# Kernel optimization log

Measured on AMD Instinct MI355X. Metric: run time of the kernel, lower is better.

Reference implementation:

```python
import jax, jax.numpy as jnp
import numpy as np

# Irreps spec: 32x0e (dim 1, with bias) + 16x1o (dim 3) + 8x2e (dim 5)
# x: [B, n_channels_in, 120] where 120 = 32*1 + 16*3 + 8*5

B = 1024
N_IN = 256
N_OUT = 256


def setup_inputs() -> dict:
    key = jax.random.key(0)
    k_x, k0, k1, k2 = jax.random.split(key, 4)
    std = 1.0 / np.sqrt(N_IN)
    x = jax.random.normal(k_x, (B, N_IN, 120), dtype=jnp.float32)
    W0 = jax.random.normal(k0, (32, N_OUT, N_IN), dtype=jnp.float32) * std
    W1 = jax.random.normal(k1, (16, N_OUT, N_IN), dtype=jnp.float32) * std
    W2 = jax.random.normal(k2, (8, N_OUT, N_IN), dtype=jnp.float32) * std
    b0 = jnp.zeros((32, N_OUT), dtype=jnp.float32)
    return {"x": x, "W0": W0, "W1": W1, "W2": W2, "b0": b0}


def reference(x, W0, W1, W2, b0):
    # Grouped form of the original per-multiplicity loop. Slices of the last
    # axis are consecutive per (irrep, multiplicity), so reshaping a group of
    # `mul` copies of an irrep of dim `d` to [..., n_in, mul, d] and doing one
    # batched einsum reproduces the original concatenation order exactly.
    groups = [(W0, 1, b0), (W1, 3, None), (W2, 5, None)]  # (weights[mul,o,i], irrep dim, bias[mul,o] or None)
    outs = []
    start = 0
    for W, d, b in groups:
        mul = W.shape[0]
        width = mul * d
        xs = x[..., start:start + width].reshape(*x.shape[:-1], mul, d)  # [..., n_in, mul, d]
        y = jnp.einsum('moi,...imd->...omd', W, xs)  # [..., n_out, mul, d]
        if b is not None:  # only l=0 irreps get a bias, broadcast over d (=1)
            y = y + b.T[:, :, None]  # [n_out, mul, 1]
        outs.append(y.reshape(*y.shape[:-2], width))  # [..., n_out, mul*d]
        start += width
    return jnp.concatenate(outs, axis=-1)  # [..., n_out, 120]
```

## Files before the change

### kernel.cpp

```cpp
#include <hip/hip_runtime.h>

typedef __attribute__((ext_vector_type(8))) short bf16x8;
typedef __attribute__((ext_vector_type(4))) float f32x4;
typedef __attribute__((ext_vector_type(8))) unsigned short u16x8;

#define DEVINL __device__ __forceinline__
#define AS1 __attribute__((address_space(1)))
#define AS3 __attribute__((address_space(3)))

constexpr int NI = 256;
constexpr int NO = 256;
constexpr int NC = 120;
constexpr int BROW = NC * NI;
constexpr int CPLANE = 1024 * NI;
constexpr int WELEMS = 56 * NO * NI;
constexpr size_t XT_ELEMS = (size_t)NC * 1024 * NI;

DEVINL ushort f2bf(float x) {
  unsigned u = __float_as_uint(x);
  u += 0x7FFFu + ((u >> 16) & 1u);
  return (ushort)(u >> 16);
}
DEVINL float bf2f(ushort v) { return __uint_as_float((unsigned)v << 16); }

__global__ __launch_bounds__(256) void prep_w(const float* __restrict__ w0,
                                              const float* __restrict__ w1,
                                              const float* __restrict__ w2,
                                              ushort* __restrict__ wb) {
  const int m = blockIdx.x >> 5;
  const int kc = blockIdx.x & 31;
  const int o = threadIdx.x;
  const float* src;
  if (m < 32)      src = w0 + ((size_t)(m * NO + o)) * NI;
  else if (m < 48) src = w1 + ((size_t)((m - 32) * NO + o)) * NI;
  else             src = w2 + ((size_t)((m - 48) * NO + o)) * NI;
  src += kc * 8;
  float4 a = *reinterpret_cast<const float4*>(src);
  float4 b = *reinterpret_cast<const float4*>(src + 4);
  u16x8 p = { f2bf(a.x), f2bf(a.y), f2bf(a.z), f2bf(a.w),
              f2bf(b.x), f2bf(b.y), f2bf(b.z), f2bf(b.w) };
  *reinterpret_cast<u16x8*>(wb + ((size_t)(blockIdx.x * 256 + o)) * 8) = p;
}

__global__ __launch_bounds__(256) void xpose(const float* __restrict__ x,
                                             ushort* __restrict__ xt) {
  __shared__ float tl[64 * 121];
  const int bid = blockIdx.x;
  const int b = bid >> 2, iq = bid & 3;
  const int t = threadIdx.x;
  const float* xb = x + (size_t)b * BROW + (size_t)iq * 64 * NC;
#pragma unroll
  for (int j = 0; j < 15; ++j) {
    const int e = (j * 256 + t) * 2;
    float2 v = *reinterpret_cast<const float2*>(xb + e);
    const int i = e / 120, c = e % 120;
    tl[i * 121 + c] = v.x;
    tl[i * 121 + c + 1] = v.y;
  }
  __syncthreads();
  ushort* dst = xt + (size_t)b * NI + iq * 64;
#pragma unroll
  for (int q = 0; q < 4; ++q) {
    const int chunk = q * 256 + t;
    if (chunk < 960) {
      const int c = chunk >> 3, ich = chunk & 7;
      u16x8 p;
#pragma unroll
      for (int k = 0; k < 8; ++k) p[k] = f2bf(tl[(ich * 8 + k) * 121 + c]);
      *reinterpret_cast<u16x8*>(dst + (size_t)c * CPLANE + ich * 8) = p;
    }
  }
}

__global__ __launch_bounds__(512, 4) void e3mixA(const ushort* __restrict__ xt,
                                                 const ushort* __restrict__ wb,
                                                 const float* __restrict__ bias0,
                                                 float* __restrict__ out) {
  __shared__ ushort xs[16640];
  const int bid = blockIdx.x;
  const int ct = bid >> 7;
  const int bt = (bid & 127) >> 2;
  const int oq = bid & 3;
  const int c0 = ct * 8, bg = bt * 32, og = oq * 64;

  const int tid = threadIdx.x, lane = tid & 63, w = tid >> 6;
  const int rb = lane & 15, rg = lane >> 4;
  const int c = c0 + w;
  const int m = c < 32 ? c : (c < 80 ? 32 + (c - 32) / 3 : 48 + (c - 80) / 5);

  const ushort* gsrc = xt + (size_t)c * CPLANE + (size_t)(bg + (lane >> 2)) * NI
                          + (((lane & 3) ^ ((lane >> 2) & 3)) * 8);

  f32x4 acc[2][4];
#pragma unroll
  for (int i = 0; i < 2; ++i)
#pragma unroll
    for (int j = 0; j < 4; ++j) acc[i][j] = (f32x4)0.0f;

#define STAGEA(BUF, S)                                                         \
  do {                                                                         \
    __builtin_amdgcn_global_load_lds((const AS1 void*)(gsrc + (S) * 32),       \
        (AS3 void*)(xs + (BUF) * 8192 + w * 1024), 16, 0, 0);                  \
    __builtin_amdgcn_global_load_lds((const AS1 void*)(gsrc + (S) * 32 + 16 * NI), \
        (AS3 void*)(xs + (BUF) * 8192 + w * 1024 + 512), 16, 0, 0);            \
  } while (0)

  STAGEA(0, 0);
  __syncthreads();

#pragma unroll 1
  for (int s = 0; s < 8; ++s) {
    if (s < 7) STAGEA((s + 1) & 1, s + 1);
    const ushort* xb = xs + (s & 1) * 8192 + w * 1024;
    bf16x8 a[2], wf[4];
#pragma unroll
    for (int fb = 0; fb < 2; ++fb)
      a[fb] = *reinterpret_cast<const bf16x8*>(
          xb + fb * 512 + rb * 32 + ((rg ^ (rb & 3)) * 8));
#pragma unroll
    for (int fo = 0; fo < 4; ++fo)
      wf[fo] = *reinterpret_cast<const bf16x8*>(
          wb + ((size_t)((m * 32 + s * 4 + rg) * NO + og + fo * 16 + rb)) * 8);
#pragma unroll
    for (int fb = 0; fb < 2; ++fb)
#pragma unroll
      for (int fo = 0; fo < 4; ++fo)
        acc[fb][fo] = __builtin_amdgcn_mfma_f32_16x16x32_bf16(a[fb], wf[fo],
                                                              acc[fb][fo], 0, 0, 0);
    __syncthreads();
  }
#undef STAGEA

  if (c0 < 32) {
#pragma unroll
    for (int fo = 0; fo < 4; ++fo) {
      const float bv = bias0[c * NO + og + fo * 16 + rb];
#pragma unroll
      for (int fb = 0; fb < 2; ++fb) acc[fb][fo] += bv;
    }
  }

#pragma unroll
  for (int fb = 0; fb < 2; ++fb)
#pragma unroll
    for (int r = 0; r < 4; ++r)
#pragma unroll
      for (int fo = 0; fo < 4; ++fo)
        xs[(fb * 16 + rg * 4 + r) * 520 + (fo * 16 + rb) * 8 + w] =
            f2bf(acc[fb][fo][r]);
  __syncthreads();
#pragma unroll
  for (int i = 0; i < 4; ++i) {
    const int g = i * 512 + tid;
    const int bp = g >> 6, o = g & 63;
    u16x8 v = *reinterpret_cast<const u16x8*>(xs + bp * 520 + o * 8);
    float4 lo = make_float4(bf2f(v[0]), bf2f(v[1]), bf2f(v[2]), bf2f(v[3]));
    float4 hi = make_float4(bf2f(v[4]), bf2f(v[5]), bf2f(v[6]), bf2f(v[7]));
    float* dst = out + ((size_t)(bg + bp) * NO + og + o) * NC + c0;
    *reinterpret_cast<float4*>(dst) = lo;
    *reinterpret_cast<float4*>(dst + 4) = hi;
  }
}

__global__ __launch_bounds__(512, 4) void e3mix2f(const float* __restrict__ x,
                                                  const ushort* __restrict__ wb,
                                                  const float* __restrict__ bias0,
                                                  float* __restrict__ out) {
  __shared__ ushort xs[8 * 16 * 64];
  const int bid = blockIdx.x;
  const int ct = bid % 15, bt = bid / 15;
  const int c0 = ct * 8, bg = bt * 16;
  const int t = threadIdx.x, lane = t & 63, wid = t >> 6;
  const int sb = lane >> 2, sp = lane & 3;
  const int rb = lane & 15, rg = lane >> 4;
  const int oc = wid * 16 + rb;
  const int srow = (wid * 16 + sb) * 64;
  const int sk0 = (sp * 16) ^ ((sb & 7) << 3);
  const int sk1 = (sp * 16 + 8) ^ ((sb & 7) << 3);

  f32x4 acc[8][2];
#pragma unroll
  for (int i = 0; i < 8; ++i) { acc[i][0] = (f32x4)0.0f; acc[i][1] = (f32x4)0.0f; }
  bf16x8 w00 = {}, w01 = {}, w10 = {}, w11 = {};

#pragma unroll 1
  for (int s = 0; s < 4; ++s) {
    if (s) __syncthreads();
    u16x8 v0, v1;
    const float* src = x + (size_t)(bg + sb) * (NI * NC)
                         + (size_t)(s * 64 + sp * 16) * NC + (c0 + wid);
#pragma unroll
    for (int jj = 0; jj < 8; ++jj) v0[jj] = f2bf(src[jj * NC]);
#pragma unroll
    for (int jj = 0; jj < 8; ++jj) v1[jj] = f2bf(src[(8 + jj) * NC]);
    *reinterpret_cast<u16x8*>(&xs[srow + sk0]) = v0;
    *reinterpret_cast<u16x8*>(&xs[srow + sk1]) = v1;
    __syncthreads();

    int mprev = -1;
#pragma unroll
    for (int cc = 0; cc < 8; ++cc) {
      const int c = c0 + cc;
      const int m = c < 32 ? c : (c < 80 ? 32 + (c - 32) / 3 : 48 + (c - 80) / 5);
      if (m != mprev) {
        const ushort* wp = wb + ((size_t)((m * 32 + s * 8 + rg) * NO + oc)) * 8;
        w00 = *reinterpret_cast<const bf16x8*>(wp);
        w10 = *reinterpret_cast<const bf16x8*>(wp + (size_t)4 * NO * 8);
        w01 = *reinterpret_cast<const bf16x8*>(wp + 128 * 8);
        w11 = *reinterpret_cast<const bf16x8*>(wp + (size_t)4 * NO * 8 + 128 * 8);
        mprev = m;
      }
      const ushort* xp = xs + (cc * 16 + rb) * 64;
      const int sz = (rb & 7) << 3;
      bf16x8 a0 = *reinterpret_cast<const bf16x8*>(xp + ((rg * 8) ^ sz));
      bf16x8 a1 = *reinterpret_cast<const bf16x8*>(xp + ((32 + rg * 8) ^ sz));
      acc[cc][0] = __builtin_amdgcn_mfma_f32_16x16x32_bf16(a0, w00, acc[cc][0], 0, 0, 0);
      acc[cc][0] = __builtin_amdgcn_mfma_f32_16x16x32_bf16(a1, w10, acc[cc][0], 0, 0, 0);
      acc[cc][1] = __builtin_amdgcn_mfma_f32_16x16x32_bf16(a0, w01, acc[cc][1], 0, 0, 0);
      acc[cc][1] = __builtin_amdgcn_mfma_f32_16x16x32_bf16(a1, w11, acc[cc][1], 0, 0, 0);
    }
  }

  if (c0 < 32) {
#pragma unroll
    for (int cc = 0; cc < 8; ++cc) {
      acc[cc][0] += bias0[(c0 + cc) * NO + oc];
      acc[cc][1] += bias0[(c0 + cc) * NO + oc + 128];
    }
  }

  const int br0 = bg + rg * 4;
#pragma unroll
  for (int of = 0; of < 2; ++of)
#pragma unroll
    for (int r = 0; r < 4; ++r) {
      float4 va = make_float4(acc[0][of][r], acc[1][of][r], acc[2][of][r], acc[3][of][r]);
      float4 vb = make_float4(acc[4][of][r], acc[5][of][r], acc[6][of][r], acc[7][of][r]);
      float* dst = out + ((size_t)(br0 + r) * NO + oc + of * 128) * NC + c0;
      *reinterpret_cast<float4*>(dst) = va;
      *reinterpret_cast<float4*>(dst + 4) = vb;
    }
}

extern "C" void kernel_launch(void* const* d_in, const int* in_sizes, int n_in,
                              void* d_out, int out_size, void* d_ws, size_t ws_size,
                              hipStream_t stream) {
  const float* x  = (const float*)d_in[0];
  const float* w0 = (const float*)d_in[1];
  const float* w1 = (const float*)d_in[2];
  const float* w2 = (const float*)d_in[3];
  const float* b0 = (const float*)d_in[4];
  float* out = (float*)d_out;
  ushort* wb = (ushort*)d_ws;
  ushort* xt = wb + WELEMS;

  prep_w<<<56 * 32, 256, 0, stream>>>(w0, w1, w2, wb);
  const bool big = ws_size >= (size_t)2 * (WELEMS + XT_ELEMS);
  if (big) {
    xpose<<<4096, 256, 0, stream>>>(x, xt);
    e3mixA<<<1920, 512, 0, stream>>>(xt, wb, b0, out);
  } else {
    e3mix2f<<<960, 512, 0, stream>>>(x, wb, b0, out);
  }
}
```

Measured before the change: 157.9 us.

## Retile mixing GEMM to 16 batch rows by full 256 outputs per block

The main mixing kernel moves from 32 batch rows by 64 outputs per block to 16 batch rows by all 256 outputs, halving the grid. Each staged x fragment is now reused across 16 output tiles and the K loop runs 4 steps of 64 instead of 8 of 32. The epilogue writes out in two halves through a larger LDS buffer. In exchange, weight fragments are loaded per wave for all 256 outputs, each wave keeps 16 accumulators, and fewer blocks are in flight.

```diff
diff --git a/kernel.cpp b/kernel.cpp
--- a/kernel.cpp
+++ b/kernel.cpp
@@ -72,93 +72,96 @@
   }
 }
 
-__global__ __launch_bounds__(512, 4) void e3mixA(const ushort* __restrict__ xt,
+__global__ __launch_bounds__(512, 4) void e3mixB(const ushort* __restrict__ xt,
                                                  const ushort* __restrict__ wb,
                                                  const float* __restrict__ bias0,
                                                  float* __restrict__ out) {
-  __shared__ ushort xs[16640];
+  __shared__ ushort xs[16448];
   const int bid = blockIdx.x;
-  const int ct = bid >> 7;
-  const int bt = (bid & 127) >> 2;
-  const int oq = bid & 3;
-  const int c0 = ct * 8, bg = bt * 32, og = oq * 64;
+  const int ct = bid >> 6;
+  const int bt = bid & 63;
+  const int c0 = ct * 8, bg = bt * 16;
 
   const int tid = threadIdx.x, lane = tid & 63, w = tid >> 6;
   const int rb = lane & 15, rg = lane >> 4;
   const int c = c0 + w;
   const int m = c < 32 ? c : (c < 80 ? 32 + (c - 32) / 3 : 48 + (c - 80) / 5);
 
-  const ushort* gsrc = xt + (size_t)c * CPLANE + (size_t)(bg + (lane >> 2)) * NI
-                          + (((lane & 3) ^ ((lane >> 2) & 3)) * 8);
-
-  f32x4 acc[2][4];
-#pragma unroll
-  for (int i = 0; i < 2; ++i)
-#pragma unroll
-    for (int j = 0; j < 4; ++j) acc[i][j] = (f32x4)0.0f;
-
-#define STAGEA(BUF, S)                                                         \
+  const int lr = lane >> 3;
+  const ushort* gsrc = xt + (size_t)c * CPLANE + (size_t)(bg + lr) * NI
+                          + ((lane & 7) ^ lr) * 8;
+
+  f32x4 acc[16];
+#pragma unroll
+  for (int i = 0; i < 16; ++i) acc[i] = (f32x4)0.0f;
+
+#define STAGEB(BUF, S)                                                         \
   do {                                                                         \
-    __builtin_amdgcn_global_load_lds((const AS1 void*)(gsrc + (S) * 32),       \
+    __builtin_amdgcn_global_load_lds((const AS1 void*)(gsrc + (S) * 64),       \
         (AS3 void*)(xs + (BUF) * 8192 + w * 1024), 16, 0, 0);                  \
-    __builtin_amdgcn_global_load_lds((const AS1 void*)(gsrc + (S) * 32 + 16 * NI), \
+    __builtin_amdgcn_global_load_lds((const AS1 void*)(gsrc + (S) * 64 + 8 * NI), \
         (AS3 void*)(xs + (BUF) * 8192 + w * 1024 + 512), 16, 0, 0);            \
   } while (0)
 
-  STAGEA(0, 0);
+  STAGEB(0, 0);
   __syncthreads();
 
 #pragma unroll 1
-  for (int s = 0; s < 8; ++s) {
-    if (s < 7) STAGEA((s + 1) & 1, s + 1);
+  for (int s = 0; s < 4; ++s) {
+    if (s < 3) STAGEB((s + 1) & 1, s + 1);
     const ushort* xb = xs + (s & 1) * 8192 + w * 1024;
-    bf16x8 a[2], wf[4];
-#pragma unroll
-    for (int fb = 0; fb < 2; ++fb)
-      a[fb] = *reinterpret_cast<const bf16x8*>(
-          xb + fb * 512 + rb * 32 + ((rg ^ (rb & 3)) * 8));
-#pragma unroll
-    for (int fo = 0; fo < 4; ++fo)
-      wf[fo] = *reinterpret_cast<const bf16x8*>(
-          wb + ((size_t)((m * 32 + s * 4 + rg) * NO + og + fo * 16 + rb)) * 8);
-#pragma unroll
-    for (int fb = 0; fb < 2; ++fb)
-#pragma unroll
-      for (int fo = 0; fo < 4; ++fo)
-        acc[fb][fo] = __builtin_amdgcn_mfma_f32_16x16x32_bf16(a[fb], wf[fo],
-                                                              acc[fb][fo], 0, 0, 0);
-    __syncthreads();
-  }
-#undef STAGEA
+#pragma unroll
+    for (int kh = 0; kh < 2; ++kh) {
+      bf16x8 a = *reinterpret_cast<const bf16x8*>(
+          xb + rb * 64 + (((kh * 4 + rg) ^ (rb & 7)) * 8));
+      const ushort* wrow = wb + ((size_t)((m * 32 + s * 8 + kh * 4 + rg) * NO + rb)) * 8;
+#pragma unroll
+      for (int h = 0; h < 2; ++h) {
+        bf16x8 wf[8];
+#pragma unroll
+        for (int j = 0; j < 8; ++j)
+          wf[j] = *reinterpret_cast<const bf16x8*>(wrow + (h * 8 + j) * 128);
+#pragma unroll
+        for (int j = 0; j < 8; ++j)
+          acc[h * 8 + j] = __builtin_amdgcn_mfma_f32_16x16x32_bf16(a, wf[j],
+                                                                   acc[h * 8 + j], 0, 0, 0);
+      }
+    }
+    __syncthreads();
+  }
+#undef STAGEB
 
   if (c0 < 32) {
 #pragma unroll
-    for (int fo = 0; fo < 4; ++fo) {
-      const float bv = bias0[c * NO + og + fo * 16 + rb];
-#pragma unroll
-      for (int fb = 0; fb < 2; ++fb) acc[fb][fo] += bv;
-    }
-  }
-
-#pragma unroll
-  for (int fb = 0; fb < 2; ++fb)
-#pragma unroll
-    for (int r = 0; r < 4; ++r)
-#pragma unroll
-      for (int fo = 0; fo < 4; ++fo)
-        xs[(fb * 16 + rg * 4 + r) * 520 + (fo * 16 + rb) * 8 + w] =
-            f2bf(acc[fb][fo][r]);
-  __syncthreads();
-#pragma unroll
-  for (int i = 0; i < 4; ++i) {
-    const int g = i * 512 + tid;
-    const int bp = g >> 6, o = g & 63;
-    u16x8 v = *reinterpret_cast<const u16x8*>(xs + bp * 520 + o * 8);
-    float4 lo = make_float4(bf2f(v[0]), bf2f(v[1]), bf2f(v[2]), bf2f(v[3]));
-    float4 hi = make_float4(bf2f(v[4]), bf2f(v[5]), bf2f(v[6]), bf2f(v[7]));
-    float* dst = out + ((size_t)(bg + bp) * NO + og + o) * NC + c0;
-    *reinterpret_cast<float4*>(dst) = lo;
-    *reinterpret_cast<float4*>(dst + 4) = hi;
+    for (int fo = 0; fo < 16; ++fo) {
+      const float bv = bias0[c * NO + fo * 16 + rb];
+      acc[fo] += bv;
+    }
+  }
+
+#pragma unroll 1
+  for (int h = 0; h < 2; ++h) {
+    __syncthreads();
+    if ((rg >> 1) == h) {
+      const int brow = (rg & 1) * 4;
+#pragma unroll
+      for (int fo = 0; fo < 16; ++fo)
+#pragma unroll
+        for (int r = 0; r < 4; ++r)
+          xs[(brow + r) * 2056 + (fo * 16 + rb) * 8 + w] = f2bf(acc[fo][r]);
+    }
+    __syncthreads();
+#pragma unroll
+    for (int i = 0; i < 4; ++i) {
+      const int g = i * 512 + tid;
+      const int bp = g >> 8, o = g & 255;
+      u16x8 v = *reinterpret_cast<const u16x8*>(xs + bp * 2056 + o * 8);
+      float4 lo = make_float4(bf2f(v[0]), bf2f(v[1]), bf2f(v[2]), bf2f(v[3]));
+      float4 hi = make_float4(bf2f(v[4]), bf2f(v[5]), bf2f(v[6]), bf2f(v[7]));
+      float* dst = out + ((size_t)(bg + h * 8 + bp) * NO + o) * NC + c0;
+      *reinterpret_cast<float4*>(dst) = lo;
+      *reinterpret_cast<float4*>(dst + 4) = hi;
+    }
   }
 }
 
@@ -258,7 +261,7 @@
   const bool big = ws_size >= (size_t)2 * (WELEMS + XT_ELEMS);
   if (big) {
     xpose<<<4096, 256, 0, stream>>>(x, xt);
-    e3mixA<<<1920, 512, 0, stream>>>(xt, wb, b0, out);
+    e3mixB<<<960, 512, 0, stream>>>(xt, wb, b0, out);
   } else {
     e3mix2f<<<960, 512, 0, stream>>>(x, wb, b0, out);
   }
```

After: 141.1 us. 1.12x faster.

## Double batch tile per block and retile transposed x layout into 64-wide k blocks

Applied to the files above, without the earlier changes.

The transpose kernel now writes x in a blocked layout (32 batch rows by 64 input channels per block), and the main GEMM kernel processes 64 batch rows per block instead of 32. Each weight fragment loaded from global is then reused across twice as many batch rows, and the grid is halved. Staging loads 64-element k chunks with an XOR swizzle, and the epilogue writes in two halves through shared memory. This doubles LDS use (64 KB) and the accumulator registers, which may lower occupancy.

```diff
diff --git a/kernel.cpp b/kernel.cpp
--- a/kernel.cpp
+++ b/kernel.cpp
@@ -58,7 +58,7 @@
     tl[i * 121 + c + 1] = v.y;
   }
   __syncthreads();
-  ushort* dst = xt + (size_t)b * NI + iq * 64;
+  ushort* dst = xt + (size_t)(b >> 5) * 8192 + (size_t)iq * 2048 + (b & 31) * 64;
 #pragma unroll
   for (int q = 0; q < 4; ++q) {
     const int chunk = q * 256 + t;
@@ -72,93 +72,105 @@
   }
 }
 
-__global__ __launch_bounds__(512, 4) void e3mixA(const ushort* __restrict__ xt,
+__global__ __launch_bounds__(512, 4) void e3mixC(const ushort* __restrict__ xt,
                                                  const ushort* __restrict__ wb,
                                                  const float* __restrict__ bias0,
                                                  float* __restrict__ out) {
-  __shared__ ushort xs[16640];
+  __shared__ ushort xs[32768];
   const int bid = blockIdx.x;
-  const int ct = bid >> 7;
-  const int bt = (bid & 127) >> 2;
+  const int ct = bid >> 6;
+  const int bt = (bid >> 2) & 15;
   const int oq = bid & 3;
-  const int c0 = ct * 8, bg = bt * 32, og = oq * 64;
+  const int c0 = ct * 8, bg = bt * 64, og = oq * 64;
 
   const int tid = threadIdx.x, lane = tid & 63, w = tid >> 6;
   const int rb = lane & 15, rg = lane >> 4;
   const int c = c0 + w;
   const int m = c < 32 ? c : (c < 80 ? 32 + (c - 32) / 3 : 48 + (c - 80) / 5);
 
-  const ushort* gsrc = xt + (size_t)c * CPLANE + (size_t)(bg + (lane >> 2)) * NI
-                          + (((lane & 3) ^ ((lane >> 2) & 3)) * 8);
-
-  f32x4 acc[2][4];
-#pragma unroll
-  for (int i = 0; i < 2; ++i)
+  const int lr = lane >> 3;
+  const ushort* gbase = xt + (size_t)c * CPLANE + (size_t)bt * 16384
+                           + lr * 64 + ((lane & 7) ^ lr) * 8;
+
+  f32x4 acc[4][4];
+#pragma unroll
+  for (int i = 0; i < 4; ++i)
 #pragma unroll
     for (int j = 0; j < 4; ++j) acc[i][j] = (f32x4)0.0f;
 
-#define STAGEA(BUF, S)                                                         \
+#define STAGEC(BUF, G)                                                         \
   do {                                                                         \
-    __builtin_amdgcn_global_load_lds((const AS1 void*)(gsrc + (S) * 32),       \
-        (AS3 void*)(xs + (BUF) * 8192 + w * 1024), 16, 0, 0);                  \
-    __builtin_amdgcn_global_load_lds((const AS1 void*)(gsrc + (S) * 32 + 16 * NI), \
-        (AS3 void*)(xs + (BUF) * 8192 + w * 1024 + 512), 16, 0, 0);            \
+    const ushort* gs_ = gbase + ((G) >> 2) * 8192 + ((G) & 3) * 2048;          \
+    ushort* ld_ = xs + (BUF) * 16384 + w * 2048;                               \
+    __builtin_amdgcn_global_load_lds((const AS1 void*)(gs_),        (AS3 void*)(ld_),        16, 0, 0); \
+    __builtin_amdgcn_global_load_lds((const AS1 void*)(gs_ + 512),  (AS3 void*)(ld_ + 512),  16, 0, 0); \
+    __builtin_amdgcn_global_load_lds((const AS1 void*)(gs_ + 1024), (AS3 void*)(ld_ + 1024), 16, 0, 0); \
+    __builtin_amdgcn_global_load_lds((const AS1 void*)(gs_ + 1536), (AS3 void*)(ld_ + 1536), 16, 0, 0); \
   } while (0)
 
-  STAGEA(0, 0);
+  STAGEC(0, 0);
   __syncthreads();
 
-#pragma unroll 1
-  for (int s = 0; s < 8; ++s) {
-    if (s < 7) STAGEA((s + 1) & 1, s + 1);
-    const ushort* xb = xs + (s & 1) * 8192 + w * 1024;
-    bf16x8 a[2], wf[4];
-#pragma unroll
-    for (int fb = 0; fb < 2; ++fb)
-      a[fb] = *reinterpret_cast<const bf16x8*>(
-          xb + fb * 512 + rb * 32 + ((rg ^ (rb & 3)) * 8));
-#pragma unroll
-    for (int fo = 0; fo < 4; ++fo)
-      wf[fo] = *reinterpret_cast<const bf16x8*>(
-          wb + ((size_t)((m * 32 + s * 4 + rg) * NO + og + fo * 16 + rb)) * 8);
-#pragma unroll
-    for (int fb = 0; fb < 2; ++fb)
+#pragma unroll
+  for (int g = 0; g < 8; ++g) {
+    if (g < 7) STAGEC((g + 1) & 1, g + 1);
+    const int bh = g >> 2, s = g & 3;
+    const ushort* p = xs + (g & 1) * 16384 + w * 2048;
+#pragma unroll
+    for (int kh = 0; kh < 2; ++kh) {
+      bf16x8 a[2], wf[4];
+#pragma unroll
+      for (int fb = 0; fb < 2; ++fb)
+        a[fb] = *reinterpret_cast<const bf16x8*>(
+            p + (fb * 16 + rb) * 64 + (((kh * 4 + rg) ^ (rb & 7)) * 8));
 #pragma unroll
       for (int fo = 0; fo < 4; ++fo)
-        acc[fb][fo] = __builtin_amdgcn_mfma_f32_16x16x32_bf16(a[fb], wf[fo],
-                                                              acc[fb][fo], 0, 0, 0);
+        wf[fo] = *reinterpret_cast<const bf16x8*>(
+            wb + ((size_t)((m * 32 + s * 8 + kh * 4 + rg) * NO
+                           + og + fo * 16 + rb)) * 8);
+#pragma unroll
+      for (int fb = 0; fb < 2; ++fb)
+#pragma unroll
+        for (int fo = 0; fo < 4; ++fo)
+          acc[bh * 2 + fb][fo] = __builtin_amdgcn_mfma_f32_16x16x32_bf16(
+              a[fb], wf[fo], acc[bh * 2 + fb][fo], 0, 0, 0);
+    }
     __syncthreads();
   }
-#undef STAGEA
-
-  if (c0 < 32) {
+#undef STAGEC
+
+  if (ct < 4) {
 #pragma unroll
     for (int fo = 0; fo < 4; ++fo) {
       const float bv = bias0[c * NO + og + fo * 16 + rb];
 #pragma unroll
-      for (int fb = 0; fb < 2; ++fb) acc[fb][fo] += bv;
-    }
-  }
-
-#pragma unroll
-  for (int fb = 0; fb < 2; ++fb)
-#pragma unroll
-    for (int r = 0; r < 4; ++r)
-#pragma unroll
-      for (int fo = 0; fo < 4; ++fo)
-        xs[(fb * 16 + rg * 4 + r) * 520 + (fo * 16 + rb) * 8 + w] =
-            f2bf(acc[fb][fo][r]);
-  __syncthreads();
-#pragma unroll
-  for (int i = 0; i < 4; ++i) {
-    const int g = i * 512 + tid;
-    const int bp = g >> 6, o = g & 63;
-    u16x8 v = *reinterpret_cast<const u16x8*>(xs + bp * 520 + o * 8);
-    float4 lo = make_float4(bf2f(v[0]), bf2f(v[1]), bf2f(v[2]), bf2f(v[3]));
-    float4 hi = make_float4(bf2f(v[4]), bf2f(v[5]), bf2f(v[6]), bf2f(v[7]));
-    float* dst = out + ((size_t)(bg + bp) * NO + og + o) * NC + c0;
-    *reinterpret_cast<float4*>(dst) = lo;
-    *reinterpret_cast<float4*>(dst + 4) = hi;
+      for (int i = 0; i < 4; ++i) acc[i][fo] += bv;
+    }
+  }
+
+#pragma unroll 1
+  for (int h = 0; h < 2; ++h) {
+    if (h) __syncthreads();
+#pragma unroll
+    for (int fb = 0; fb < 2; ++fb)
+#pragma unroll
+      for (int r = 0; r < 4; ++r)
+#pragma unroll
+        for (int fo = 0; fo < 4; ++fo)
+          xs[(fb * 16 + rg * 4 + r) * 520 + (fo * 16 + rb) * 8 + w] =
+              f2bf(acc[h * 2 + fb][fo][r]);
+    __syncthreads();
+#pragma unroll
+    for (int i = 0; i < 4; ++i) {
+      const int g = i * 512 + tid;
+      const int bp = g >> 6, o = g & 63;
+      u16x8 v = *reinterpret_cast<const u16x8*>(xs + bp * 520 + o * 8);
+      float4 lo = make_float4(bf2f(v[0]), bf2f(v[1]), bf2f(v[2]), bf2f(v[3]));
+      float4 hi = make_float4(bf2f(v[4]), bf2f(v[5]), bf2f(v[6]), bf2f(v[7]));
+      float* dst = out + ((size_t)(bg + h * 32 + bp) * NO + og + o) * NC + c0;
+      *reinterpret_cast<float4*>(dst) = lo;
+      *reinterpret_cast<float4*>(dst + 4) = hi;
+    }
   }
 }
 
@@ -258,7 +270,7 @@
   const bool big = ws_size >= (size_t)2 * (WELEMS + XT_ELEMS);
   if (big) {
     xpose<<<4096, 256, 0, stream>>>(x, xt);
-    e3mixA<<<1920, 512, 0, stream>>>(xt, wb, b0, out);
+    e3mixC<<<960, 512, 0, stream>>>(xt, wb, b0, out);
   } else {
     e3mix2f<<<960, 512, 0, stream>>>(x, wb, b0, out);
   }
```

Result: slower. 298.8 us (+89.3%).
